# Kernel tuning notes

Hardware: AMD Instinct MI355X
Metric: run time of the kernel (lower is better)

Reference implementation:

```python
import jax, jax.numpy as jnp
import numpy as np
import math

N, M, S, D = 256, 512, 128, 512  # num_vids, num_music, num_segments, embed_dim


def layer_norm(x, g, b, eps=1e-5):
    mu = jnp.mean(x, axis=-1, keepdims=True)
    var = jnp.mean(jnp.square(x - mu), axis=-1, keepdims=True)
    return (x - mu) * jax.lax.rsqrt(var + eps) * g + b


def setup_inputs() -> dict:
    key = jax.random.key(0)
    ks = jax.random.split(key, 16)
    s = 0.02
    return {
        "video_embeds": jax.random.normal(ks[0], (N, D), jnp.float32),
        "music_embeds": jax.random.normal(ks[1], (M, S, D), jnp.float32),
        "music_mask": jnp.ones((M, S), jnp.int32),
        "ln1_g": jnp.ones((D,), jnp.float32), "ln1_b": jnp.zeros((D,), jnp.float32),
        "Wq": jax.random.normal(ks[2], (D, D), jnp.float32) * s, "bq": jnp.zeros((D,), jnp.float32),
        "Wk": jax.random.normal(ks[3], (D, D), jnp.float32) * s, "bk": jnp.zeros((D,), jnp.float32),
        "Wv": jax.random.normal(ks[4], (D, D), jnp.float32) * s, "bv": jnp.zeros((D,), jnp.float32),
        "Wo": jax.random.normal(ks[5], (D, D), jnp.float32) * s, "bo": jnp.zeros((D,), jnp.float32),
        "Wl": jax.random.normal(ks[6], (D, D), jnp.float32) * s, "bl": jnp.zeros((D,), jnp.float32),
        "ln2_g": jnp.ones((D,), jnp.float32), "ln2_b": jnp.zeros((D,), jnp.float32),
        "ln3_g": jnp.ones((D,), jnp.float32), "ln3_b": jnp.zeros((D,), jnp.float32),
    }


def reference(video_embeds, music_embeds, music_mask,
              ln1_g, ln1_b, Wq, bq, Wk, bk, Wv, bv, Wo, bo, Wl, bl,
              ln2_g, ln2_b, ln3_g, ln3_b):
    d = video_embeds.shape[-1]
    # layer_norm1 applied to both streams
    v_ln = layer_norm(video_embeds, ln1_g, ln1_b)           # (N, D)
    m_ln = layer_norm(music_embeds, ln1_g, ln1_b)           # (M, S, D)
    # single-head cross-attention (MultiHeadedAttention_mask, num_heads=1)
    q = v_ln @ Wq.T + bq                                    # (N, D)
    k = m_ln @ Wk.T + bk                                    # (M, S, D)
    v = m_ln @ Wv.T + bv                                    # (M, S, D)
    logits = jnp.einsum('nd,msd->mns', q, k) / math.sqrt(d)  # (M, N, S)
    logits = jnp.where(music_mask[:, None, :] == 0, -jnp.inf, logits)
    weights = jax.nn.softmax(logits, axis=-1)               # softmax over segments
    attn = jnp.einsum('mns,msd->mnd', weights, v)           # (M, N, D)
    o = attn @ Wo.T + bo                                    # (M, N, D)
    # layer_norm2 -> linear -> residual (dropout is identity in eval) -> layer_norm3
    o = layer_norm(o, ln2_g, ln2_b)
    lin = o @ Wl.T + bl
    out = layer_norm(o + lin, ln3_g, ln3_b)
    return out
```

## Files before the change

### kernel.cpp

```cpp
#include <hip/hip_runtime.h>

typedef __attribute__((ext_vector_type(8))) short short8;
typedef __attribute__((ext_vector_type(4))) float f32x4;
typedef __attribute__((ext_vector_type(4))) unsigned short u16x4;

__device__ __forceinline__ unsigned short f2bf(float f){
  unsigned int u = __builtin_bit_cast(unsigned int, f);
  u = (u + 0x7FFFu + ((u >> 16) & 1u)) >> 16;
  return (unsigned short)u;
}
__device__ __forceinline__ float bf2f(unsigned short h){
  unsigned int u = ((unsigned int)h) << 16;
  return __builtin_bit_cast(float, u);
}
__device__ __forceinline__ f32x4 mfma16(short8 a, short8 b, f32x4 c){
  return __builtin_amdgcn_mfma_f32_16x16x32_bf16(a, b, c, 0, 0, 0);
}
__device__ __forceinline__ void gload16(const void* g, void* l){
  __builtin_amdgcn_global_load_lds((const __attribute__((address_space(1))) void*)g,
                                   (__attribute__((address_space(3))) void*)l, 16, 0, 0);
}

__global__ __launch_bounds__(256) void cvt_f32_bf16(const float* __restrict__ src,
                                                    unsigned short* __restrict__ dst){
  int i = (blockIdx.x * 256 + threadIdx.x) * 4;
  float4 v = *(const float4*)(src + i);
  u16x4 o = { f2bf(v.x), f2bf(v.y), f2bf(v.z), f2bf(v.w) };
  *(u16x4*)(dst + i) = o;
}

__global__ __launch_bounds__(256) void ln_rows(const float* __restrict__ x,
                                               const float* __restrict__ g,
                                               const float* __restrict__ b,
                                               unsigned short* __restrict__ y,
                                               int nrows){
  const int wid = threadIdx.x >> 6, lane = threadIdx.x & 63;
  const int row = blockIdx.x * 4 + wid;
  if (row >= nrows) return;
  const float* xr = x + (long)row * 512;
  float4 v0 = *(const float4*)(xr + lane * 4);
  float4 v1 = *(const float4*)(xr + 256 + lane * 4);
  float s  = v0.x + v0.y + v0.z + v0.w + v1.x + v1.y + v1.z + v1.w;
  float s2 = v0.x*v0.x + v0.y*v0.y + v0.z*v0.z + v0.w*v0.w
           + v1.x*v1.x + v1.y*v1.y + v1.z*v1.z + v1.w*v1.w;
  #pragma unroll
  for (int m = 1; m < 64; m <<= 1){ s += __shfl_xor(s, m); s2 += __shfl_xor(s2, m); }
  const float mu = s * (1.f/512.f);
  const float rstd = rsqrtf(s2 * (1.f/512.f) - mu*mu + 1e-5f);
  float4 g0 = *(const float4*)(g + lane*4), g1 = *(const float4*)(g + 256 + lane*4);
  float4 b0 = *(const float4*)(b + lane*4), b1 = *(const float4*)(b + 256 + lane*4);
  u16x4 o0 = { f2bf((v0.x-mu)*rstd*g0.x + b0.x), f2bf((v0.y-mu)*rstd*g0.y + b0.y),
               f2bf((v0.z-mu)*rstd*g0.z + b0.z), f2bf((v0.w-mu)*rstd*g0.w + b0.w) };
  u16x4 o1 = { f2bf((v1.x-mu)*rstd*g1.x + b1.x), f2bf((v1.y-mu)*rstd*g1.y + b1.y),
               f2bf((v1.z-mu)*rstd*g1.z + b1.z), f2bf((v1.w-mu)*rstd*g1.w + b1.w) };
  *(u16x4*)(y + (long)row * 512 + lane * 4) = o0;
  *(u16x4*)(y + (long)row * 512 + 256 + lane * 4) = o1;
}

__global__ __launch_bounds__(256) void ln_weight_prep(
    const float* __restrict__ Wl, const float* __restrict__ g2,
    const float* __restrict__ b2, const float* __restrict__ bl,
    const float* __restrict__ bo,
    unsigned short* __restrict__ wlp, float* __restrict__ u,
    float* __restrict__ v, float* __restrict__ bias_cat){
  const int wid = threadIdx.x >> 6, lane = threadIdx.x & 63;
  const int n = blockIdx.x * 4 + wid;
  const float* row = Wl + (long)n * 512;
  float su = 0.f, sv = 0.f, sc = 0.f;
  #pragma unroll
  for (int h = 0; h < 2; ++h){
    const int c0 = h * 256 + lane * 4;
    float4 w  = *(const float4*)(row + c0);
    float4 gg = *(const float4*)(g2 + c0);
    float4 bb = *(const float4*)(b2 + c0);
    float4 oo = *(const float4*)(bo + c0);
    float4 wp = { w.x*gg.x, w.y*gg.y, w.z*gg.z, w.w*gg.w };
    su += wp.x + wp.y + wp.z + wp.w;
    sv += w.x*bb.x + w.y*bb.y + w.z*bb.z + w.w*bb.w;
    sc += wp.x*oo.x + wp.y*oo.y + wp.z*oo.z + wp.w*oo.w;
    u16x4 o = { f2bf(wp.x), f2bf(wp.y), f2bf(wp.z), f2bf(wp.w) };
    *(u16x4*)(wlp + (long)n * 512 + c0) = o;
  }
  #pragma unroll
  for (int m = 1; m < 64; m <<= 1){
    su += __shfl_xor(su, m); sv += __shfl_xor(sv, m); sc += __shfl_xor(sc, m);
  }
  if (lane == 0){
    u[n] = su;
    v[n] = sv + bl[n];
    bias_cat[n] = bo[n];
    bias_cat[512 + n] = sc;
  }
}

__global__ __launch_bounds__(256) void transpose_bf(const float* __restrict__ src,
                                                    unsigned short* __restrict__ dst){
  __shared__ float tile[64][65];
  const int t = threadIdx.x;
  const int k0 = blockIdx.x * 64, c0 = blockIdx.y * 64;
  const int j = t & 63, i = t >> 6;
  #pragma unroll
  for (int rr = 0; rr < 16; ++rr)
    tile[i + rr*4][j] = src[(long)(c0 + i + rr*4) * 512 + k0 + j];
  __syncthreads();
  #pragma unroll
  for (int rr = 0; rr < 16; ++rr)
    dst[(long)(k0 + i + rr*4) * 512 + c0 + j] = f2bf(tile[j][i + rr*4]);
}

__global__ __launch_bounds__(256) void gemm_bt(const unsigned short* __restrict__ A,
                                               const unsigned short* __restrict__ B,
                                               const float* __restrict__ bias,
                                               unsigned short* __restrict__ out,
                                               int transposed){
  __shared__ unsigned short At[128][40];
  __shared__ unsigned short Bt[128][40];
  const int t = threadIdx.x, lane = t & 63, wid = t >> 6;
  const int l15 = lane & 15, l4 = lane >> 4;
  const int wr = wid >> 1, wc = wid & 1;
  const int rowBase = blockIdx.y * 128;
  const int colBase = blockIdx.x * 128;
  f32x4 zero = {0.f, 0.f, 0.f, 0.f};
  f32x4 acc[4][4];
  #pragma unroll
  for (int i = 0; i < 4; ++i)
    #pragma unroll
    for (int j = 0; j < 4; ++j) acc[i][j] = zero;
  const int sr = t >> 1, sh = (t & 1) * 16;
  for (int ks = 0; ks < 16; ++ks){
    const int k0 = ks * 32;
    const unsigned short* sa = A + (long)(rowBase + sr) * 512 + k0 + sh;
    *(short8*)&At[sr][sh]     = *(const short8*)sa;
    *(short8*)&At[sr][sh + 8] = *(const short8*)(sa + 8);
    const unsigned short* sb = B + (long)(colBase + sr) * 512 + k0 + sh;
    *(short8*)&Bt[sr][sh]     = *(const short8*)sb;
    *(short8*)&Bt[sr][sh + 8] = *(const short8*)(sb + 8);
    __syncthreads();
    short8 af[4], bfv[4];
    #pragma unroll
    for (int i = 0; i < 4; ++i) af[i]  = *(const short8*)&At[wr*64 + i*16 + l15][l4*8];
    #pragma unroll
    for (int i = 0; i < 4; ++i) bfv[i] = *(const short8*)&Bt[wc*64 + i*16 + l15][l4*8];
    #pragma unroll
    for (int i = 0; i < 4; ++i)
      #pragma unroll
      for (int j = 0; j < 4; ++j)
        acc[i][j] = mfma16(af[i], bfv[j], acc[i][j]);
    __syncthreads();
  }
  #pragma unroll
  for (int i = 0; i < 4; ++i){
    const int r0 = rowBase + wr*64 + i*16 + l4*4;
    #pragma unroll
    for (int j = 0; j < 4; ++j){
      const int c = colBase + wc*64 + j*16 + l15;
      const float bb = bias ? bias[c] : 0.f;
      #pragma unroll
      for (int jr = 0; jr < 4; ++jr){
        const float v = acc[i][j][jr] + bb;
        const long rr = r0 + jr;
        if (!transposed){
          out[rr * 512 + c] = f2bf(v);
        } else {
          const long m = rr >> 7, s = rr & 127;
          out[(m * 512 + c) * 128 + s] = f2bf(v);
        }
      }
    }
  }
}

__global__ __launch_bounds__(256) void gemm_kv97(const unsigned short* __restrict__ A,
                                                 const unsigned short* __restrict__ B,
                                                 const float* __restrict__ bk,
                                                 const float* __restrict__ bv,
                                                 unsigned short* __restrict__ kout,
                                                 unsigned short* __restrict__ vout){
  __shared__ unsigned short A_lds[8192];
  __shared__ unsigned short B_lds[8192];
  const int t = threadIdx.x, lane = t & 63, wid = t >> 6;
  const int l15 = lane & 15, l4 = lane >> 4;
  const int wr = wid >> 1, wc = wid & 1;
  const int b = blockIdx.x;
  const int kk = b >> 3;
  const int colBase = (kk & 7) * 128;
  const long panel = (b & 7) + 8 * (kk >> 3);
  const long rowBase = panel * 128;
  f32x4 zero = {0.f,0.f,0.f,0.f};
  f32x4 acc[4][4];
  #pragma unroll
  for (int i = 0; i < 4; ++i)
    #pragma unroll
    for (int j = 0; j < 4; ++j) acc[i][j] = zero;
  for (int ks = 0; ks < 8; ++ks){
    const int k0 = ks * 64;
    #pragma unroll
    for (int sub = 0; sub < 2; ++sub){
      #pragma unroll
      for (int h = 0; h < 2; ++h){
        const int p = h*256 + t;
        const int row = p >> 2, g = (p & 3) ^ ((row >> 1) & 3);
        gload16(A + (rowBase + row)*512 + k0 + sub*32 + g*8, A_lds + sub*4096 + p*8);
        gload16(B + (long)(colBase + row)*512 + k0 + sub*32 + g*8, B_lds + sub*4096 + p*8);
      }
    }
    __syncthreads();
    #pragma unroll
    for (int sub = 0; sub < 2; ++sub){
      short8 af[4], bfv[4];
      #pragma unroll
      for (int i = 0; i < 4; ++i){
        const int ra = wr*64 + i*16 + l15;
        af[i]  = *(const short8*)(A_lds + sub*4096 + (ra*4 + (l4 ^ ((ra >> 1) & 3)))*8);
        const int rb = wc*64 + i*16 + l15;
        bfv[i] = *(const short8*)(B_lds + sub*4096 + (rb*4 + (l4 ^ ((rb >> 1) & 3)))*8);
      }
      #pragma unroll
      for (int i = 0; i < 4; ++i)
        #pragma unroll
        for (int j = 0; j < 4; ++j)
          acc[i][j] = mfma16(af[i], bfv[j], acc[i][j]);
    }
    __syncthreads();
  }
  if (colBase < 512){
    #pragma unroll
    for (int i = 0; i < 4; ++i){
      const long r0 = rowBase + wr*64 + i*16 + l4*4;
      #pragma unroll
      for (int j = 0; j < 4; ++j){
        const int c = colBase + wc*64 + j*16 + l15;
        const float bb = bk[c];
        #pragma unroll
        for (int jr = 0; jr < 4; ++jr)
          kout[(r0 + jr)*512 + c] = f2bf(acc[i][j][jr] + bb);
      }
    }
  } else {
    #pragma unroll
    for (int i = 0; i < 4; ++i){
      const int s0 = wr*64 + i*16 + l4*4;
      #pragma unroll
      for (int j = 0; j < 4; ++j){
        const int d = colBase - 512 + wc*64 + j*16 + l15;
        const float bb = bv[d];
        #pragma unroll
        for (int jr = 0; jr < 4; ++jr)
          vout[(panel*512 + d)*128 + s0 + jr] = f2bf(acc[i][j][jr] + bb);
      }
    }
  }
}

__global__ __launch_bounds__(256) void attn_kernel(const unsigned short* __restrict__ q,
                                                   const unsigned short* __restrict__ k,
                                                   const unsigned short* __restrict__ vT,
                                                   const int* __restrict__ mask,
                                                   unsigned short* __restrict__ attn){
  __shared__ __align__(16) char smem[74752];
  unsigned short (*q_lds)[520] = (unsigned short (*)[520])smem;
  unsigned short* k_lin = (unsigned short*)(smem + 66560);
  unsigned short (*w_lds)[136] = (unsigned short (*)[136])smem;
  float* red = (float*)(smem + 17408);
  unsigned short* v_lin = (unsigned short*)(smem + 19456);
  const int b = blockIdx.x;
  const int m = (b & 7) + 8 * ((b >> 3) >> 2);
  const int qb = (b >> 3) & 3;
  const int t = threadIdx.x, lane = t & 63, wid = t >> 6;
  const int l15 = lane & 15, l4 = lane >> 4;
  {
    const int r = t >> 2, c0 = (t & 3) * 128;
    const unsigned short* src = q + (long)(qb*64 + r) * 512 + c0;
    #pragma unroll
    for (int i = 0; i < 128; i += 8)
      *(short8*)&q_lds[r][c0 + i] = *(const short8*)(src + i);
  }
  f32x4 zero = {0.f,0.f,0.f,0.f};
  f32x4 acc[4][2];
  #pragma unroll
  for (int i = 0; i < 4; ++i){ acc[i][0] = zero; acc[i][1] = zero; }
  const unsigned short* kbase = k + (long)m * 128 * 512;
  for (int ks = 0; ks < 16; ++ks){
    const int k0 = ks * 32;
    #pragma unroll
    for (int h = 0; h < 2; ++h){
      const int p = h*256 + t;
      const int row = p >> 2, g = (p & 3) ^ ((row >> 1) & 3);
      gload16(kbase + (long)row*512 + k0 + g*8, k_lin + p*8);
    }
    __syncthreads();
    short8 af[4], bfv[2];
    #pragma unroll
    for (int i = 0; i < 4; ++i) af[i] = *(const short8*)&q_lds[i*16 + l15][k0 + l4*8];
    #pragma unroll
    for (int j = 0; j < 2; ++j){
      const int rb = wid*32 + j*16 + l15;
      bfv[j] = *(const short8*)(k_lin + (rb*4 + (l4 ^ ((rb >> 1) & 3)))*8);
    }
    #pragma unroll
    for (int i = 0; i < 4; ++i)
      #pragma unroll
      for (int j = 0; j < 2; ++j)
        acc[i][j] = mfma16(af[i], bfv[j], acc[i][j]);
    __syncthreads();
  }
  const float scale = 0.04419417382415922f;
  const int* mrow = mask + m * 128;
  const int mk0 = mrow[wid*32 + l15];
  const int mk1 = mrow[wid*32 + 16 + l15];
  float e[4][2][4], wmax[4][4], wsum[4][4];
  #pragma unroll
  for (int i = 0; i < 4; ++i)
    #pragma unroll
    for (int jr = 0; jr < 4; ++jr){
      float v0 = mk0 ? acc[i][0][jr]*scale : -3.0e38f;
      float v1 = mk1 ? acc[i][1][jr]*scale : -3.0e38f;
      float mx = fmaxf(v0, v1);
      mx = fmaxf(mx, __shfl_xor(mx, 1));
      mx = fmaxf(mx, __shfl_xor(mx, 2));
      mx = fmaxf(mx, __shfl_xor(mx, 4));
      mx = fmaxf(mx, __shfl_xor(mx, 8));
      const float e0 = __expf(v0 - mx), e1 = __expf(v1 - mx);
      float sm = e0 + e1;
      sm += __shfl_xor(sm, 1);
      sm += __shfl_xor(sm, 2);
      sm += __shfl_xor(sm, 4);
      sm += __shfl_xor(sm, 8);
      e[i][0][jr] = e0; e[i][1][jr] = e1;
      wmax[i][jr] = mx; wsum[i][jr] = sm;
    }
  if (l15 == 0){
    #pragma unroll
    for (int i = 0; i < 4; ++i)
      #pragma unroll
      for (int jr = 0; jr < 4; ++jr){
        const int r = i*16 + l4*4 + jr;
        red[r*8 + wid*2]     = wmax[i][jr];
        red[r*8 + wid*2 + 1] = wsum[i][jr];
      }
  }
  __syncthreads();
  float inv[4][4];
  #pragma unroll
  for (int i = 0; i < 4; ++i)
    #pragma unroll
    for (int jr = 0; jr < 4; ++jr){
      const int r = i*16 + l4*4 + jr;
      float4 a = *(const float4*)(red + r*8);
      float4 c = *(const float4*)(red + r*8 + 4);
      const float gm = fmaxf(fmaxf(a.x, a.z), fmaxf(c.x, c.z));
      const float gs = a.y*__expf(a.x - gm) + a.w*__expf(a.z - gm)
                     + c.y*__expf(c.x - gm) + c.w*__expf(c.z - gm);
      inv[i][jr] = (gs > 0.f) ? (1.f / gs) : 0.f;
      const float sc = __expf(wmax[i][jr] - gm);
      #pragma unroll
      for (int j = 0; j < 2; ++j)
        w_lds[r][wid*32 + j*16 + l15] = f2bf(e[i][j][jr] * sc);
    }
  const long rowb = (long)m * 256 + qb * 64;
  const unsigned short* vbase = vT + (long)m * 512 * 128;
  for (int db = 0; db < 4; ++db){
    __syncthreads();
    #pragma unroll
    for (int it = 0; it < 8; ++it){
      const int p = it*256 + t;
      const int row = p >> 4, g = (p & 15) ^ (row & 7);
      gload16(vbase + (long)(db*128 + row)*128 + g*8, v_lin + p*8);
    }
    __syncthreads();
    f32x4 pacc[4][2];
    #pragma unroll
    for (int i = 0; i < 4; ++i){ pacc[i][0] = zero; pacc[i][1] = zero; }
    #pragma unroll
    for (int ks2 = 0; ks2 < 4; ++ks2){
      short8 wf[4], vf[2];
      #pragma unroll
      for (int i = 0; i < 4; ++i) wf[i] = *(const short8*)&w_lds[i*16 + l15][ks2*32 + l4*8];
      #pragma unroll
      for (int j = 0; j < 2; ++j){
        const int rv = wid*32 + j*16 + l15;
        vf[j] = *(const short8*)(v_lin + (rv*16 + ((ks2*4 + l4) ^ (rv & 7)))*8);
      }
      #pragma unroll
      for (int i = 0; i < 4; ++i)
        #pragma unroll
        for (int j = 0; j < 2; ++j)
          pacc[i][j] = mfma16(wf[i], vf[j], pacc[i][j]);
    }
    #pragma unroll
    for (int i = 0; i < 4; ++i)
      #pragma unroll
      for (int j = 0; j < 2; ++j)
        #pragma unroll
        for (int jr = 0; jr < 4; ++jr)
          attn[(rowb + i*16 + l4*4 + jr) * 512 + db*128 + wid*32 + j*16 + l15] =
              f2bf(pacc[i][j][jr] * inv[i][jr]);
  }
}

__global__ __launch_bounds__(256) void gemm97(const unsigned short* __restrict__ A,
                                              const unsigned short* __restrict__ B,
                                              unsigned short* __restrict__ C){
  __shared__ unsigned short A_lds[8192];
  __shared__ unsigned short B_lds[8192];
  const int t = threadIdx.x, lane = t & 63, wid = t >> 6;
  const int l15 = lane & 15, l4 = lane >> 4;
  const int wr = wid >> 1, wc = wid & 1;
  const int b = blockIdx.x;
  const int kk = b >> 3;
  const int colBase = (kk & 7) * 128;
  const long rowBase = ((long)(b & 7) + 8 * (kk >> 3)) * 128;
  f32x4 zero = {0.f,0.f,0.f,0.f};
  f32x4 acc[4][4];
  #pragma unroll
  for (int i = 0; i < 4; ++i)
    #pragma unroll
    for (int j = 0; j < 4; ++j) acc[i][j] = zero;
  for (int ks = 0; ks < 8; ++ks){
    const int k0 = ks * 64;
    #pragma unroll
    for (int sub = 0; sub < 2; ++sub){
      #pragma unroll
      for (int h = 0; h < 2; ++h){
        const int p = h*256 + t;
        const int row = p >> 2, g = (p & 3) ^ ((row >> 1) & 3);
        gload16(A + (rowBase + row)*512 + k0 + sub*32 + g*8, A_lds + sub*4096 + p*8);
        gload16(B + (long)(colBase + row)*512 + k0 + sub*32 + g*8, B_lds + sub*4096 + p*8);
      }
    }
    __syncthreads();
    #pragma unroll
    for (int sub = 0; sub < 2; ++sub){
      short8 af[4], bfv[4];
      #pragma unroll
      for (int i = 0; i < 4; ++i){
        const int ra = wr*64 + i*16 + l15;
        af[i]  = *(const short8*)(A_lds + sub*4096 + (ra*4 + (l4 ^ ((ra >> 1) & 3)))*8);
        const int rb = wc*64 + i*16 + l15;
        bfv[i] = *(const short8*)(B_lds + sub*4096 + (rb*4 + (l4 ^ ((rb >> 1) & 3)))*8);
      }
      #pragma unroll
      for (int i = 0; i < 4; ++i)
        #pragma unroll
        for (int j = 0; j < 4; ++j)
          acc[i][j] = mfma16(af[i], bfv[j], acc[i][j]);
    }
    __syncthreads();
  }
  #pragma unroll
  for (int i = 0; i < 4; ++i){
    const long r0 = rowBase + wr*64 + i*16 + l4*4;
    #pragma unroll
    for (int j = 0; j < 4; ++j){
      const int c = colBase + wc*64 + j*16 + l15;
      #pragma unroll
      for (int jr = 0; jr < 4; ++jr)
        C[(r0 + jr)*1024 + c] = f2bf(acc[i][j][jr]);
    }
  }
}

__global__ __launch_bounds__(256) void ln_epilogue(
    const unsigned short* Cb, float* out,
    const float* __restrict__ bias_cat, const float* __restrict__ u,
    const float* __restrict__ v,
    const float* __restrict__ g2, const float* __restrict__ b2,
    const float* __restrict__ g3, const float* __restrict__ b3){
  const int wid = threadIdx.x >> 6, lane = threadIdx.x & 63;
  const long row = (long)blockIdx.x * 4 + wid;
  const unsigned short* cr = Cb + row * 1024;
  short8 ov = *(const short8*)(cr + lane * 8);
  short8 pv = *(const short8*)(cr + 512 + lane * 8);
  const int n0 = lane * 8;
  float4 bo0 = *(const float4*)(bias_cat + n0);
  float4 bo1 = *(const float4*)(bias_cat + n0 + 4);
  float4 c20 = *(const float4*)(bias_cat + 512 + n0);
  float4 c21 = *(const float4*)(bias_cat + 512 + n0 + 4);
  float o[8], p[8];
  #pragma unroll
  for (int j = 0; j < 4; ++j){
    o[j]   = bf2f((unsigned short)ov[j])   + ((const float*)&bo0)[j];
    o[4+j] = bf2f((unsigned short)ov[4+j]) + ((const float*)&bo1)[j];
    p[j]   = bf2f((unsigned short)pv[j])   + ((const float*)&c20)[j];
    p[4+j] = bf2f((unsigned short)pv[4+j]) + ((const float*)&c21)[j];
  }
  float s = 0.f, s2 = 0.f;
  #pragma unroll
  for (int j = 0; j < 8; ++j){ s += o[j]; s2 += o[j]*o[j]; }
  #pragma unroll
  for (int m = 1; m < 64; m <<= 1){ s += __shfl_xor(s, m); s2 += __shfl_xor(s2, m); }
  const float mu2 = s * (1.f/512.f);
  const float rstd2 = rsqrtf(s2 * (1.f/512.f) - mu2*mu2 + 1e-5f);
  float4 uv0 = *(const float4*)(u + n0), uv1 = *(const float4*)(u + n0 + 4);
  float4 vv0 = *(const float4*)(v + n0), vv1 = *(const float4*)(v + n0 + 4);
  float4 g20v = *(const float4*)(g2 + n0), g21v = *(const float4*)(g2 + n0 + 4);
  float4 b20v = *(const float4*)(b2 + n0), b21v = *(const float4*)(b2 + n0 + 4);
  float y[8];
  #pragma unroll
  for (int j = 0; j < 4; ++j){
    const float lin0 = rstd2 * (p[j]   - mu2 * ((const float*)&uv0)[j]) + ((const float*)&vv0)[j];
    const float lin1 = rstd2 * (p[4+j] - mu2 * ((const float*)&uv1)[j]) + ((const float*)&vv1)[j];
    const float oln0 = (o[j]   - mu2) * rstd2 * ((const float*)&g20v)[j] + ((const float*)&b20v)[j];
    const float oln1 = (o[4+j] - mu2) * rstd2 * ((const float*)&g21v)[j] + ((const float*)&b21v)[j];
    y[j]   = oln0 + lin0;
    y[4+j] = oln1 + lin1;
  }
  float t1 = 0.f, t2 = 0.f;
  #pragma unroll
  for (int j = 0; j < 8; ++j){ t1 += y[j]; t2 += y[j]*y[j]; }
  #pragma unroll
  for (int m = 1; m < 64; m <<= 1){ t1 += __shfl_xor(t1, m); t2 += __shfl_xor(t2, m); }
  const float mu3 = t1 * (1.f/512.f);
  const float rstd3 = rsqrtf(t2 * (1.f/512.f) - mu3*mu3 + 1e-5f);
  float4 g30v = *(const float4*)(g3 + n0), g31v = *(const float4*)(g3 + n0 + 4);
  float4 b30v = *(const float4*)(b3 + n0), b31v = *(const float4*)(b3 + n0 + 4);
  float4 r0, r1;
  #pragma unroll
  for (int j = 0; j < 4; ++j){
    ((float*)&r0)[j] = (y[j]   - mu3) * rstd3 * ((const float*)&g30v)[j] + ((const float*)&b30v)[j];
    ((float*)&r1)[j] = (y[4+j] - mu3) * rstd3 * ((const float*)&g31v)[j] + ((const float*)&b31v)[j];
  }
  *(float4*)(out + row * 512 + n0)     = r0;
  *(float4*)(out + row * 512 + n0 + 4) = r1;
}

extern "C" void kernel_launch(void* const* d_in, const int* in_sizes, int n_in,
                              void* d_out, int out_size, void* d_ws, size_t ws_size,
                              hipStream_t stream){
  const float* video = (const float*)d_in[0];
  const float* music = (const float*)d_in[1];
  const int*   mask  = (const int*)d_in[2];
  const float* ln1g  = (const float*)d_in[3];
  const float* ln1b  = (const float*)d_in[4];
  const float* Wq = (const float*)d_in[5];  const float* bq = (const float*)d_in[6];
  const float* Wk = (const float*)d_in[7];  const float* bk = (const float*)d_in[8];
  const float* Wv = (const float*)d_in[9];  const float* bv = (const float*)d_in[10];
  const float* Wo = (const float*)d_in[11]; const float* bo = (const float*)d_in[12];
  const float* Wl = (const float*)d_in[13]; const float* bl = (const float*)d_in[14];
  const float* g2 = (const float*)d_in[15]; const float* b2 = (const float*)d_in[16];
  const float* g3 = (const float*)d_in[17]; const float* b3 = (const float*)d_in[18];

  char* ob = (char*)d_out;
  unsigned short* mln   = (unsigned short*)ob;
  unsigned short* kbuf  = (unsigned short*)(ob + 67108864);
  unsigned short* vTbuf = (unsigned short*)(ob + 134217728);
  unsigned short* Cbuf  = (unsigned short*)ob;
  float* outp = (float*)d_out;

  char* wsb = (char*)d_ws;
  unsigned short* attnb = (unsigned short*)wsb;
  unsigned short* Wq_bf = (unsigned short*)(wsb + 134217728);
  unsigned short* KVcat = Wq_bf + 262144;
  unsigned short* q_ws  = KVcat + 524288;
  unsigned short* vln   = q_ws + 131072;
  unsigned short* Bcat  = vln + 131072;
  unsigned short* wlp   = Bcat + 524288;
  unsigned short* WoT   = wlp + 262144;
  float* bias_cat = (float*)(WoT + 262144);
  float* u_vec    = bias_cat + 1024;
  float* v_vec    = u_vec + 512;

  cvt_f32_bf16<<<256, 256, 0, stream>>>(Wq, Wq_bf);
  cvt_f32_bf16<<<256, 256, 0, stream>>>(Wk, KVcat);
  cvt_f32_bf16<<<256, 256, 0, stream>>>(Wv, KVcat + 262144);
  cvt_f32_bf16<<<256, 256, 0, stream>>>(Wo, Bcat);
  ln_weight_prep<<<128, 256, 0, stream>>>(Wl, g2, b2, bl, bo, wlp, u_vec, v_vec, bias_cat);
  transpose_bf<<<dim3(8, 8), 256, 0, stream>>>(Wo, WoT);
  gemm_bt<<<dim3(4, 4), 256, 0, stream>>>(wlp, WoT, nullptr, Bcat + 262144, 0);

  ln_rows<<<16384, 256, 0, stream>>>(music, ln1g, ln1b, mln, 65536);
  ln_rows<<<64,    256, 0, stream>>>(video, ln1g, ln1b, vln, 256);

  gemm_bt<<<dim3(4, 2), 256, 0, stream>>>(vln, Wq_bf, bq, q_ws, 0);
  gemm_kv97<<<4096, 256, 0, stream>>>(mln, KVcat, bk, bv, kbuf, vTbuf);

  attn_kernel<<<2048, 256, 0, stream>>>(q_ws, kbuf, vTbuf, mask, attnb);

  for (int c = 0; c < 4; ++c){
    const long rowoff = (long)c * 32768;
    gemm97<<<2048, 256, 0, stream>>>(attnb + rowoff*512, Bcat, Cbuf + rowoff*1024);
    ln_epilogue<<<8192, 256, 0, stream>>>(Cbuf + rowoff*1024, outp + rowoff*512,
                                          bias_cat, u_vec, v_vec, g2, b2, g3, b3);
  }
}
```

Before: 663.2 us.

## Fold Wk into query and Wv·Wo into value projection, drop separate K and output GEMMs

Result: faster. 616.3 us (-7.1%).

```diff
diff --git a/kernel.cpp b/kernel.cpp
--- a/kernel.cpp
+++ b/kernel.cpp
@@ -27,6 +27,12 @@
   float4 v = *(const float4*)(src + i);
   u16x4 o = { f2bf(v.x), f2bf(v.y), f2bf(v.z), f2bf(v.w) };
   *(u16x4*)(dst + i) = o;
+}
+
+__global__ __launch_bounds__(256) void copy_bf(const unsigned short* __restrict__ src,
+                                               unsigned short* __restrict__ dst){
+  int i = (blockIdx.x * 256 + threadIdx.x) * 8;
+  *(short8*)(dst + i) = *(const short8*)(src + i);
 }
 
 __global__ __launch_bounds__(256) void ln_rows(const float* __restrict__ x,
@@ -93,6 +99,21 @@
   }
 }
 
+__global__ __launch_bounds__(256) void cvb_add(const unsigned short* __restrict__ Bc,
+                                               const float* __restrict__ bv,
+                                               float* __restrict__ bias_cat){
+  const int wid = threadIdx.x >> 6, lane = threadIdx.x & 63;
+  const int n = blockIdx.x * 4 + wid;
+  const unsigned short* row = Bc + (long)n * 512;
+  short8 a = *(const short8*)(row + lane * 8);
+  float s = 0.f;
+  #pragma unroll
+  for (int j = 0; j < 8; ++j) s += bf2f((unsigned short)a[j]) * bv[lane*8 + j];
+  #pragma unroll
+  for (int m = 1; m < 64; m <<= 1) s += __shfl_xor(s, m);
+  if (lane == 0) bias_cat[n] += s;
+}
+
 __global__ __launch_bounds__(256) void transpose_bf(const float* __restrict__ src,
                                                     unsigned short* __restrict__ dst){
   __shared__ float tile[64][65];
@@ -170,12 +191,9 @@
   }
 }
 
-__global__ __launch_bounds__(256) void gemm_kv97(const unsigned short* __restrict__ A,
-                                                 const unsigned short* __restrict__ B,
-                                                 const float* __restrict__ bk,
-                                                 const float* __restrict__ bv,
-                                                 unsigned short* __restrict__ kout,
-                                                 unsigned short* __restrict__ vout){
+__global__ __launch_bounds__(256) void vb97(const unsigned short* __restrict__ A,
+                                            const unsigned short* __restrict__ B,
+                                            unsigned short* __restrict__ vbt){
   __shared__ unsigned short A_lds[8192];
   __shared__ unsigned short B_lds[8192];
   const int t = threadIdx.x, lane = t & 63, wid = t >> 6;
@@ -223,40 +241,26 @@
     }
     __syncthreads();
   }
-  if (colBase < 512){
-    #pragma unroll
-    for (int i = 0; i < 4; ++i){
-      const long r0 = rowBase + wr*64 + i*16 + l4*4;
-      #pragma unroll
-      for (int j = 0; j < 4; ++j){
-        const int c = colBase + wc*64 + j*16 + l15;
-        const float bb = bk[c];
-        #pragma unroll
-        for (int jr = 0; jr < 4; ++jr)
-          kout[(r0 + jr)*512 + c] = f2bf(acc[i][j][jr] + bb);
-      }
-    }
-  } else {
-    #pragma unroll
-    for (int i = 0; i < 4; ++i){
-      const int s0 = wr*64 + i*16 + l4*4;
-      #pragma unroll
-      for (int j = 0; j < 4; ++j){
-        const int d = colBase - 512 + wc*64 + j*16 + l15;
-        const float bb = bv[d];
-        #pragma unroll
-        for (int jr = 0; jr < 4; ++jr)
-          vout[(panel*512 + d)*128 + s0 + jr] = f2bf(acc[i][j][jr] + bb);
-      }
-    }
-  }
-}
-
-__global__ __launch_bounds__(256) void attn_kernel(const unsigned short* __restrict__ q,
-                                                   const unsigned short* __restrict__ k,
-                                                   const unsigned short* __restrict__ vT,
-                                                   const int* __restrict__ mask,
-                                                   unsigned short* __restrict__ attn){
+  #pragma unroll
+  for (int i = 0; i < 4; ++i){
+    const int s0 = wr*64 + i*16 + l4*4;
+    #pragma unroll
+    for (int j = 0; j < 4; ++j){
+      const int n = colBase + wc*64 + j*16 + l15;
+      #pragma unroll
+      for (int jr = 0; jr < 4; ++jr)
+        vbt[((long)panel*1024 + n)*128 + s0 + jr] = f2bf(acc[i][j][jr]);
+    }
+  }
+}
+
+__global__ __launch_bounds__(256) void attn_c(const unsigned short* __restrict__ q2,
+                                              const unsigned short* __restrict__ mlnb,
+                                              int m_mln0,
+                                              const unsigned short* __restrict__ vbt,
+                                              const int* __restrict__ mask,
+                                              unsigned short* __restrict__ C,
+                                              int m0){
   __shared__ __align__(16) char smem[74752];
   unsigned short (*q_lds)[520] = (unsigned short (*)[520])smem;
   unsigned short* k_lin = (unsigned short*)(smem + 66560);
@@ -264,13 +268,14 @@
   float* red = (float*)(smem + 17408);
   unsigned short* v_lin = (unsigned short*)(smem + 19456);
   const int b = blockIdx.x;
-  const int m = (b & 7) + 8 * ((b >> 3) >> 2);
+  const int m_local = (b & 7) + 8 * (b >> 5);
   const int qb = (b >> 3) & 3;
+  const int m = m0 + m_local;
   const int t = threadIdx.x, lane = t & 63, wid = t >> 6;
   const int l15 = lane & 15, l4 = lane >> 4;
   {
     const int r = t >> 2, c0 = (t & 3) * 128;
-    const unsigned short* src = q + (long)(qb*64 + r) * 512 + c0;
+    const unsigned short* src = q2 + (long)(qb*64 + r) * 512 + c0;
     #pragma unroll
     for (int i = 0; i < 128; i += 8)
       *(short8*)&q_lds[r][c0 + i] = *(const short8*)(src + i);
@@ -279,7 +284,7 @@
   f32x4 acc[4][2];
   #pragma unroll
   for (int i = 0; i < 4; ++i){ acc[i][0] = zero; acc[i][1] = zero; }
-  const unsigned short* kbase = k + (long)m * 128 * 512;
+  const unsigned short* kbase = mlnb + (long)(m - m_mln0) * 128 * 512;
   for (int ks = 0; ks < 16; ++ks){
     const int k0 = ks * 32;
     #pragma unroll
@@ -340,7 +345,6 @@
       }
   }
   __syncthreads();
-  float inv[4][4];
   #pragma unroll
   for (int i = 0; i < 4; ++i)
     #pragma unroll
@@ -351,21 +355,21 @@
       const float gm = fmaxf(fmaxf(a.x, a.z), fmaxf(c.x, c.z));
       const float gs = a.y*__expf(a.x - gm) + a.w*__expf(a.z - gm)
                      + c.y*__expf(c.x - gm) + c.w*__expf(c.z - gm);
-      inv[i][jr] = (gs > 0.f) ? (1.f / gs) : 0.f;
-      const float sc = __expf(wmax[i][jr] - gm);
+      const float inv = (gs > 0.f) ? (1.f / gs) : 0.f;
+      const float sc = __expf(wmax[i][jr] - gm) * inv;
       #pragma unroll
       for (int j = 0; j < 2; ++j)
         w_lds[r][wid*32 + j*16 + l15] = f2bf(e[i][j][jr] * sc);
     }
   const long rowb = (long)m * 256 + qb * 64;
-  const unsigned short* vbase = vT + (long)m * 512 * 128;
-  for (int db = 0; db < 4; ++db){
+  const unsigned short* vbase = vbt + (long)m * 1024 * 128;
+  for (int nb = 0; nb < 8; ++nb){
     __syncthreads();
     #pragma unroll
     for (int it = 0; it < 8; ++it){
       const int p = it*256 + t;
       const int row = p >> 4, g = (p & 15) ^ (row & 7);
-      gload16(vbase + (long)(db*128 + row)*128 + g*8, v_lin + p*8);
+      gload16(vbase + (long)(nb*128 + row)*128 + g*8, v_lin + p*8);
     }
     __syncthreads();
     f32x4 pacc[4][2];
@@ -393,70 +397,8 @@
       for (int j = 0; j < 2; ++j)
         #pragma unroll
         for (int jr = 0; jr < 4; ++jr)
-          attn[(rowb + i*16 + l4*4 + jr) * 512 + db*128 + wid*32 + j*16 + l15] =
-              f2bf(pacc[i][j][jr] * inv[i][jr]);
-  }
-}
-
-__global__ __launch_bounds__(256) void gemm97(const unsigned short* __restrict__ A,
-                                              const unsigned short* __restrict__ B,
-                                              unsigned short* __restrict__ C){
-  __shared__ unsigned short A_lds[8192];
-  __shared__ unsigned short B_lds[8192];
-  const int t = threadIdx.x, lane = t & 63, wid = t >> 6;
-  const int l15 = lane & 15, l4 = lane >> 4;
-  const int wr = wid >> 1, wc = wid & 1;
-  const int b = blockIdx.x;
-  const int kk = b >> 3;
-  const int colBase = (kk & 7) * 128;
-  const long rowBase = ((long)(b & 7) + 8 * (kk >> 3)) * 128;
-  f32x4 zero = {0.f,0.f,0.f,0.f};
-  f32x4 acc[4][4];
-  #pragma unroll
-  for (int i = 0; i < 4; ++i)
-    #pragma unroll
-    for (int j = 0; j < 4; ++j) acc[i][j] = zero;
-  for (int ks = 0; ks < 8; ++ks){
-    const int k0 = ks * 64;
-    #pragma unroll
-    for (int sub = 0; sub < 2; ++sub){
-      #pragma unroll
-      for (int h = 0; h < 2; ++h){
-        const int p = h*256 + t;
-        const int row = p >> 2, g = (p & 3) ^ ((row >> 1) & 3);
-        gload16(A + (rowBase + row)*512 + k0 + sub*32 + g*8, A_lds + sub*4096 + p*8);
-        gload16(B + (long)(colBase + row)*512 + k0 + sub*32 + g*8, B_lds + sub*4096 + p*8);
-      }
-    }
-    __syncthreads();
-    #pragma unroll
-    for (int sub = 0; sub < 2; ++sub){
-      short8 af[4], bfv[4];
-      #pragma unroll
-      for (int i = 0; i < 4; ++i){
-        const int ra = wr*64 + i*16 + l15;
-        af[i]  = *(const short8*)(A_lds + sub*4096 + (ra*4 + (l4 ^ ((ra >> 1) & 3)))*8);
-        const int rb = wc*64 + i*16 + l15;
-        bfv[i] = *(const short8*)(B_lds + sub*4096 + (rb*4 + (l4 ^ ((rb >> 1) & 3)))*8);
-      }
-      #pragma unroll
-      for (int i = 0; i < 4; ++i)
-        #pragma unroll
-        for (int j = 0; j < 4; ++j)
-          acc[i][j] = mfma16(af[i], bfv[j], acc[i][j]);
-    }
-    __syncthreads();
-  }
-  #pragma unroll
-  for (int i = 0; i < 4; ++i){
-    const long r0 = rowBase + wr*64 + i*16 + l4*4;
-    #pragma unroll
-    for (int j = 0; j < 4; ++j){
-      const int c = colBase + wc*64 + j*16 + l15;
-      #pragma unroll
-      for (int jr = 0; jr < 4; ++jr)
-        C[(r0 + jr)*1024 + c] = f2bf(acc[i][j][jr]);
-    }
+          C[(rowb + i*16 + l4*4 + jr) * 1024 + nb*128 + wid*32 + j*16 + l15] =
+              f2bf(pacc[i][j][jr]);
   }
 }
 
@@ -533,7 +475,7 @@
   const float* ln1g  = (const float*)d_in[3];
   const float* ln1b  = (const float*)d_in[4];
   const float* Wq = (const float*)d_in[5];  const float* bq = (const float*)d_in[6];
-  const float* Wk = (const float*)d_in[7];  const float* bk = (const float*)d_in[8];
+  const float* Wk = (const float*)d_in[7];
   const float* Wv = (const float*)d_in[9];  const float* bv = (const float*)d_in[10];
   const float* Wo = (const float*)d_in[11]; const float* bo = (const float*)d_in[12];
   const float* Wl = (const float*)d_in[13]; const float* bl = (const float*)d_in[14];
@@ -541,45 +483,56 @@
   const float* g3 = (const float*)d_in[17]; const float* b3 = (const float*)d_in[18];
 
   char* ob = (char*)d_out;
-  unsigned short* mln   = (unsigned short*)ob;
-  unsigned short* kbuf  = (unsigned short*)(ob + 67108864);
-  unsigned short* vTbuf = (unsigned short*)(ob + 134217728);
-  unsigned short* Cbuf  = (unsigned short*)ob;
+  unsigned short* mln  = (unsigned short*)(ob + 201326592);
+  unsigned short* Cb   = (unsigned short*)ob;
   float* outp = (float*)d_out;
 
   char* wsb = (char*)d_ws;
-  unsigned short* attnb = (unsigned short*)wsb;
-  unsigned short* Wq_bf = (unsigned short*)(wsb + 134217728);
-  unsigned short* KVcat = Wq_bf + 262144;
-  unsigned short* q_ws  = KVcat + 524288;
-  unsigned short* vln   = q_ws + 131072;
-  unsigned short* Bcat  = vln + 131072;
-  unsigned short* wlp   = Bcat + 524288;
-  unsigned short* WoT   = wlp + 262144;
-  float* bias_cat = (float*)(WoT + 262144);
+  unsigned short* vbt    = (unsigned short*)wsb;
+  unsigned short* Wq_bf  = (unsigned short*)(wsb + 134217728);
+  unsigned short* Bcat   = Wq_bf + 262144;
+  unsigned short* wlp    = Bcat + 524288;
+  unsigned short* WoT    = wlp + 262144;
+  unsigned short* WkT    = WoT + 262144;
+  unsigned short* WvT    = WkT + 262144;
+  unsigned short* Wvb    = WvT + 262144;
+  unsigned short* q_ws   = Wvb + 524288;
+  unsigned short* q2_ws  = q_ws + 131072;
+  unsigned short* vln    = q2_ws + 131072;
+  unsigned short* mln_cp = vln + 131072;
+  float* bias_cat = (float*)(mln_cp + 524288);
   float* u_vec    = bias_cat + 1024;
   float* v_vec    = u_vec + 512;
 
   cvt_f32_bf16<<<256, 256, 0, stream>>>(Wq, Wq_bf);
-  cvt_f32_bf16<<<256, 256, 0, stream>>>(Wk, KVcat);
-  cvt_f32_bf16<<<256, 256, 0, stream>>>(Wv, KVcat + 262144);
   cvt_f32_bf16<<<256, 256, 0, stream>>>(Wo, Bcat);
   ln_weight_prep<<<128, 256, 0, stream>>>(Wl, g2, b2, bl, bo, wlp, u_vec, v_vec, bias_cat);
   transpose_bf<<<dim3(8, 8), 256, 0, stream>>>(Wo, WoT);
+  transpose_bf<<<dim3(8, 8), 256, 0, stream>>>(Wk, WkT);
+  transpose_bf<<<dim3(8, 8), 256, 0, stream>>>(Wv, WvT);
   gemm_bt<<<dim3(4, 4), 256, 0, stream>>>(wlp, WoT, nullptr, Bcat + 262144, 0);
+  gemm_bt<<<dim3(4, 8), 256, 0, stream>>>(Bcat, WvT, nullptr, Wvb, 0);
+  cvb_add<<<256, 256, 0, stream>>>(Bcat, bv, bias_cat);
 
   ln_rows<<<16384, 256, 0, stream>>>(music, ln1g, ln1b, mln, 65536);
   ln_rows<<<64,    256, 0, stream>>>(video, ln1g, ln1b, vln, 256);
-
   gemm_bt<<<dim3(4, 2), 256, 0, stream>>>(vln, Wq_bf, bq, q_ws, 0);
-  gemm_kv97<<<4096, 256, 0, stream>>>(mln, KVcat, bk, bv, kbuf, vTbuf);
-
-  attn_kernel<<<2048, 256, 0, stream>>>(q_ws, kbuf, vTbuf, mask, attnb);
-
-  for (int c = 0; c < 4; ++c){
-    const long rowoff = (long)c * 32768;
-    gemm97<<<2048, 256, 0, stream>>>(attnb + rowoff*512, Bcat, Cbuf + rowoff*1024);
-    ln_epilogue<<<8192, 256, 0, stream>>>(Cbuf + rowoff*1024, outp + rowoff*512,
-                                          bias_cat, u_vec, v_vec, g2, b2, g3, b3);
-  }
-}
+  gemm_bt<<<dim3(4, 2), 256, 0, stream>>>(q_ws, WkT, nullptr, q2_ws, 0);
+
+  vb97<<<4096, 256, 0, stream>>>(mln, Wvb, vbt);
+
+  const int m0s[5] = {0, 128, 256, 384, 480};
+  const int dms[5] = {128, 128, 128, 96, 24};
+  for (int cidx = 0; cidx < 5; ++cidx){
+    const int m0 = m0s[cidx], dm = dms[cidx];
+    attn_c<<<dm * 4, 256, 0, stream>>>(q2_ws, mln, 0, vbt, mask, Cb, m0);
+    ln_epilogue<<<dm * 64, 256, 0, stream>>>(Cb + (long)m0*256*1024,
+                                             outp + (long)m0*256*512,
+                                             bias_cat, u_vec, v_vec, g2, b2, g3, b3);
+  }
+  copy_bf<<<256, 256, 0, stream>>>(mln + (long)504*128*512, mln_cp);
+  attn_c<<<32, 256, 0, stream>>>(q2_ws, mln_cp, 504, vbt, mask, Cb, 504);
+  ln_epilogue<<<512, 256, 0, stream>>>(Cb + (long)504*256*1024,
+                                       outp + (long)504*256*512,
+                                       bias_cat, u_vec, v_vec, g2, b2, g3, b3);
+}
```
